# Kernel optimization log

Hardware: AMD Instinct MI355X
Metric: run time of the kernel (lower is better)

## Reference

```python
import jax, jax.numpy as jnp
import numpy as np

B, T, D = 32, 1024, 1024  # batch, t_k (encoder steps), attn_sz == cell_state_sz


def setup_inputs() -> dict:
    key = jax.random.key(0)
    ks = jax.random.split(key, 7)
    scale = 1.0 / np.sqrt(D)
    return {
        "h_i": jax.random.normal(ks[0], (B, T, D), jnp.float32),
        "s_t": jax.random.normal(ks[1], (B, D), jnp.float32),
        "coverage": jax.random.uniform(ks[2], (B, T), jnp.float32),
        "W_h": jax.random.normal(ks[3], (D, D), jnp.float32) * scale,
        "W_s": jax.random.normal(ks[4], (D, D), jnp.float32) * scale,
        "b_s": jnp.zeros((D,), jnp.float32),
        "W_c": jax.random.normal(ks[5], (D,), jnp.float32) * scale,  # Dense(1 -> D) kernel
        "V_w": jax.random.normal(ks[6], (D,), jnp.float32) * scale,  # Dense(D -> 1) kernel
    }


def reference(h_i, s_t, coverage, W_h, W_s, b_s, W_c, V_w):
    # enc_features = W_h(h_i): (B, T, D)
    enc_features = jnp.einsum("btd,de->bte", h_i, W_h)
    # dec_features = W_s(s_t) broadcast over time: (B, 1, D)
    dec_features = (s_t @ W_s + b_s)[:, None, :]
    # coverage features: scalar coverage per step times (1->D) kernel
    cov_features = coverage[:, :, None] * W_c[None, None, :]
    features = enc_features + dec_features + cov_features
    # e_t = V(tanh(features)) squeezed to (B, T)
    e_t = jnp.einsum("btd,d->bt", jnp.tanh(features), V_w)
    a_t = jax.nn.softmax(e_t, axis=1)
    coverage_new = coverage + a_t
    # context = a_t @ h_i : (B, D)
    context_vector = jnp.einsum("bt,btd->bd", a_t, h_i)
    return context_vector, a_t, coverage_new
```

## Files before the change

kernel.cpp:

```cpp
#include <hip/hip_runtime.h>

#define B_ 32
#define T_ 1024
#define D_ 1024
#define M_ (B_ * T_)
#define NT_ 8
#define NT2 4
#define BM_ 128
#define BN_ 128
#define BK_ 64
#define NKT (D_ / BK_)
#define LSTR 72

#define FENCE_ALL() asm volatile("s_waitcnt vmcnt(0) lgkmcnt(0)" ::: "memory")

typedef __attribute__((ext_vector_type(8))) short short8;
typedef __attribute__((ext_vector_type(4))) float f32x4;

__device__ __forceinline__ unsigned f2bf(float f) {
    union { float f; unsigned u; } v; v.f = f;
    return (v.u + 0x7FFFu + ((v.u >> 16) & 1u)) >> 16;
}
__device__ __forceinline__ unsigned pack2(float a, float b) {
    return f2bf(a) | (f2bf(b) << 16);
}
__device__ __forceinline__ float bf2f(unsigned hi16) {
    union { unsigned u; float f; } v; v.u = hi16 << 16;
    return v.f;
}
__device__ __forceinline__ float fast_tanh(float x) {
    x = fminf(15.0f, fmaxf(-15.0f, x));
    float e = __expf(2.0f * x);
    return (e - 1.0f) * __fdividef(1.0f, e + 1.0f);
}

#define PREP_CONVH_BLKS 2048
#define PREP_CONVWT_BLKS 256
#define PREP_DEC_BLKS (B_ * 16)
__global__ __launch_bounds__(256) void prep_kernel(
    const float* __restrict__ h_i, uint4* __restrict__ h_bf4,
    const float* __restrict__ W_h, unsigned short* __restrict__ Wt,
    const float* __restrict__ s_t, const float* __restrict__ W_s,
    const float* __restrict__ b_s, float* __restrict__ dec_part)
{
    __shared__ float smem[64 * 65];
    const int bid = blockIdx.x;
    const int tid = threadIdx.x;
    if (bid < PREP_CONVH_BLKS) {
        const int idx = bid * 256 + tid;
        const int stride = PREP_CONVH_BLKS * 256;
        const int ngroups = M_ * D_ / 8;
        const float4* in4 = (const float4*)h_i;
        for (int g = idx; g < ngroups; g += stride) {
            const float4 a = in4[2 * g];
            const float4 b = in4[2 * g + 1];
            h_bf4[g] = make_uint4(pack2(a.x, a.y), pack2(a.z, a.w),
                                  pack2(b.x, b.y), pack2(b.z, b.w));
        }
    } else if (bid < PREP_CONVH_BLKS + PREP_CONVWT_BLKS) {
        const int tb = bid - PREP_CONVH_BLKS;
        float (*tile)[65] = (float (*)[65])smem;
        const int k0 = (tb & 15) * 64;
        const int n0 = (tb >> 4) * 64;
        const int tx = tid & 63, ty = tid >> 6;
#pragma unroll
        for (int r = 0; r < 16; ++r) {
            const int row = ty * 16 + r;
            tile[row][tx] = W_h[(size_t)(k0 + row) * D_ + n0 + tx];
        }
        __syncthreads();
#pragma unroll
        for (int r = 0; r < 16; ++r) {
            const int row = ty * 16 + r;
            Wt[(size_t)(n0 + row) * D_ + k0 + tx] = (unsigned short)f2bf(tile[tx][row]);
        }
    } else {
        const int db = bid - (PREP_CONVH_BLKS + PREP_CONVWT_BLKS);
        const int kc = db & 3;
        const int nc = (db >> 2) & 3;
        const int b  = db >> 4;
        const int d = nc * 256 + tid;
        const int k0 = kc * 256;
        float* s_lds = smem;
        s_lds[tid] = s_t[b * D_ + k0 + tid];
        __syncthreads();
        float acc = (kc == 0) ? b_s[d] : 0.f;
#pragma unroll 8
        for (int k = 0; k < 256; ++k) acc += s_lds[k] * W_s[(size_t)(k0 + k) * D_ + d];
        dec_part[kc * (B_ * D_) + b * D_ + d] = acc;
    }
}

__global__ __launch_bounds__(512, 2) void attn_gemm2(
    const unsigned short* __restrict__ h_bf, const unsigned short* __restrict__ wt_bf,
    const float* __restrict__ dec_part, const float* __restrict__ coverage,
    const float* __restrict__ W_c, const float* __restrict__ V_w,
    float* __restrict__ e_part)
{
    __shared__ __align__(16) unsigned short lds2[2][2][256 * 64];
    __shared__ float e_red[4][256];

    const int tid = threadIdx.x;
    const int nt2 = blockIdx.x >> 7;
    const int mt  = blockIdx.x & 127;
    const int m0 = mt * 256;
    const int n0 = nt2 * 256;
    const int bb = m0 >> 10;

    const int wave = tid >> 6;
    const int lane = tid & 63;
    const int wr = wave >> 2;
    const int wc = wave & 3;
    const int lr = lane & 15;
    const int lk = lane >> 4;

    f32x4 acc[8][4];
    const f32x4 fzero = {0.f, 0.f, 0.f, 0.f};
#pragma unroll
    for (int i = 0; i < 8; ++i)
#pragma unroll
        for (int j = 0; j < 4; ++j) acc[i][j] = fzero;

    const char* gA = (const char*)h_bf + (size_t)m0 * (D_ * 2);
    const char* gB = (const char*)wt_bf + (size_t)n0 * (D_ * 2);
    const int lrow8 = lane >> 3;
    const int scol = (((lane & 7) ^ lrow8) << 4);
    const int sw = (lr & 7) << 4;

#define STAGE2(buf, kt)                                                            \
    {                                                                              \
        _Pragma("unroll")                                                          \
        for (int j = 0; j < 4; ++j) {                                              \
            const int c = wave * 4 + j;                                            \
            const int row = c * 8 + lrow8;                                         \
            const size_t goff = (size_t)row * (D_ * 2) + (size_t)(kt) * 128 + scol;\
            __builtin_amdgcn_global_load_lds(                                      \
                (const __attribute__((address_space(1))) void*)(gA + goff),        \
                (__attribute__((address_space(3))) void*)((char*)lds2 +            \
                    ((buf) * 2 + 0) * 32768 + c * 1024), 16, 0, 0);                \
            __builtin_amdgcn_global_load_lds(                                      \
                (const __attribute__((address_space(1))) void*)(gB + goff),        \
                (__attribute__((address_space(3))) void*)((char*)lds2 +            \
                    ((buf) * 2 + 1) * 32768 + c * 1024), 16, 0, 0);                \
        }                                                                          \
    }

    STAGE2(0, 0);
    FENCE_ALL();
    __syncthreads();

    short8 aA[4][2];
    short8 bB[4][2];

#define LOADA(g)                                                                   \
    _Pragma("unroll")                                                              \
    for (int mi = 0; mi < 4; ++mi)                                                 \
        _Pragma("unroll")                                                          \
        for (int kk = 0; kk < 2; ++kk)                                             \
            aA[mi][kk] = *(const short8*)(ldsA +                                   \
                (wr * 128 + ((g) * 4 + mi) * 16 + lr) * 128 +                      \
                (((kk) * 64 + lk * 16) ^ sw));

#define LOADB(pair)                                                                \
    _Pragma("unroll")                                                              \
    for (int nn = 0; nn < 2; ++nn)                                                 \
        _Pragma("unroll")                                                          \
        for (int kk = 0; kk < 2; ++kk)                                             \
            bB[(pair) * 2 + nn][kk] = *(const short8*)(ldsB +                      \
                (wc * 64 + ((pair) * 2 + nn) * 16 + lr) * 128 +                    \
                (((kk) * 64 + lk * 16) ^ sw));

#define MFMA_Q(goff, npair)                                                        \
    __builtin_amdgcn_s_setprio(1);                                                 \
    _Pragma("unroll")                                                              \
    for (int mi = 0; mi < 4; ++mi)                                                 \
        _Pragma("unroll")                                                          \
        for (int nn = 0; nn < 2; ++nn)                                             \
            _Pragma("unroll")                                                      \
            for (int kk = 0; kk < 2; ++kk)                                         \
                acc[(goff) + mi][(npair) * 2 + nn] =                               \
                    __builtin_amdgcn_mfma_f32_16x16x32_bf16(                       \
                        aA[mi][kk], bB[(npair) * 2 + nn][kk],                      \
                        acc[(goff) + mi][(npair) * 2 + nn], 0, 0, 0);              \
    __builtin_amdgcn_s_setprio(0);

    for (int kt = 0; kt < NKT; ++kt) {
        const int cur = kt & 1;
        const char* ldsA = (const char*)lds2 + (cur * 2 + 0) * 32768;
        const char* ldsB = (const char*)lds2 + (cur * 2 + 1) * 32768;

        if (kt + 1 < NKT) STAGE2(cur ^ 1, kt + 1);
        LOADA(0);
        LOADB(0);
        MFMA_Q(0, 0);
        __builtin_amdgcn_s_barrier();

        LOADB(1);
        MFMA_Q(0, 1);
        __builtin_amdgcn_s_barrier();

        LOADA(1);
        MFMA_Q(4, 1);
        __builtin_amdgcn_s_barrier();

        MFMA_Q(4, 0);
        FENCE_ALL();
        __syncthreads();
    }
#undef STAGE2
#undef LOADA
#undef LOADB
#undef MFMA_Q

    float esum[8][4];
    float covv[8][4];
#pragma unroll
    for (int mi = 0; mi < 8; ++mi)
#pragma unroll
        for (int r = 0; r < 4; ++r) {
            esum[mi][r] = 0.f;
            covv[mi][r] = coverage[m0 + wr * 128 + mi * 16 + lk * 4 + r];
        }
    const float* dp = dec_part + bb * D_;
#pragma unroll
    for (int ni = 0; ni < 4; ++ni) {
        const int n = n0 + wc * 64 + ni * 16 + lr;
        const float vw = V_w[n];
        const float dc = dp[n] + dp[B_ * D_ + n] + dp[2 * B_ * D_ + n] + dp[3 * B_ * D_ + n];
        const float wcv = W_c[n];
#pragma unroll
        for (int mi = 0; mi < 8; ++mi)
#pragma unroll
            for (int r = 0; r < 4; ++r) {
                const float f = acc[mi][ni][r] + dc + covv[mi][r] * wcv;
                esum[mi][r] += fast_tanh(f) * vw;
            }
    }
#pragma unroll
    for (int off = 1; off <= 8; off <<= 1)
#pragma unroll
        for (int mi = 0; mi < 8; ++mi)
#pragma unroll
            for (int r = 0; r < 4; ++r)
                esum[mi][r] += __shfl_xor(esum[mi][r], off, 64);

    if (lr == 0) {
#pragma unroll
        for (int mi = 0; mi < 8; ++mi)
#pragma unroll
            for (int r = 0; r < 4; ++r)
                e_red[wc][wr * 128 + mi * 16 + lk * 4 + r] = esum[mi][r];
    }
    FENCE_ALL();
    __syncthreads();
    if (tid < 256)
        e_part[(size_t)nt2 * M_ + m0 + tid] =
            e_red[0][tid] + e_red[1][tid] + e_red[2][tid] + e_red[3][tid];
}

__global__ __launch_bounds__(256, 2) void attn_gemm_kernel(
    const float* __restrict__ h_i, const float* __restrict__ W_h,
    const float* __restrict__ dec_part, const float* __restrict__ coverage,
    const float* __restrict__ W_c, const float* __restrict__ V_w,
    float* __restrict__ e_part)
{
    __shared__ __align__(16) unsigned short lA[BM_][LSTR];
    __shared__ __align__(16) unsigned short lB[BN_][LSTR];
    __shared__ float e_red[256];

    const int tid = threadIdx.x;
    const int nt = blockIdx.x >> 8;
    const int mt = blockIdx.x & 255;
    const int m0 = mt * BM_;
    const int n0 = nt * BN_;
    const int bb = m0 >> 10;

    const int wave = tid >> 6;
    const int lane = tid & 63;
    const int wr = wave >> 1, wc = wave & 1;
    const int lr = lane & 15;
    const int lk = lane >> 4;

    f32x4 acc[4][4];
    const f32x4 fzero = {0.f, 0.f, 0.f, 0.f};
#pragma unroll
    for (int i = 0; i < 4; ++i)
#pragma unroll
        for (int j = 0; j < 4; ++j) acc[i][j] = fzero;

    const int a_row = tid >> 4;
    const int a_k = (tid & 15) << 2;
    const float* hA = h_i + (size_t)m0 * D_;

    for (int k0 = 0; k0 < D_; k0 += BK_) {
#pragma unroll
        for (int p = 0; p < 8; ++p) {
            const int row = a_row + p * 16;
            const float4 v = *(const float4*)(hA + (size_t)row * D_ + (k0 + a_k));
            *(uint2*)&lA[row][a_k] = make_uint2(pack2(v.x, v.y), pack2(v.z, v.w));
        }
#pragma unroll
        for (int p = 0; p < 8; ++p) {
            const int task = tid + p * 256;
            const int n = task & 127;
            const int kg = task >> 7;
            const float* wp = W_h + (size_t)(k0 + kg * 4) * D_ + n0 + n;
            const float x0 = wp[0 * D_], x1 = wp[1 * D_], x2 = wp[2 * D_], x3 = wp[3 * D_];
            *(uint2*)&lB[n][kg * 4] = make_uint2(pack2(x0, x1), pack2(x2, x3));
        }
        __syncthreads();

        short8 af[2][4], bfr[2][4];
#pragma unroll
        for (int kk = 0; kk < 2; ++kk)
#pragma unroll
            for (int i = 0; i < 4; ++i) {
                af[kk][i]  = *(const short8*)&lA[wr * 64 + i * 16 + lr][kk * 32 + lk * 8];
                bfr[kk][i] = *(const short8*)&lB[wc * 64 + i * 16 + lr][kk * 32 + lk * 8];
            }
#pragma unroll
        for (int kk = 0; kk < 2; ++kk)
#pragma unroll
            for (int mi = 0; mi < 4; ++mi)
#pragma unroll
                for (int ni = 0; ni < 4; ++ni)
                    acc[mi][ni] = __builtin_amdgcn_mfma_f32_16x16x32_bf16(
                        af[kk][mi], bfr[kk][ni], acc[mi][ni], 0, 0, 0);
        __syncthreads();
    }

    float esum[4][4];
    float covv[4][4];
#pragma unroll
    for (int mi = 0; mi < 4; ++mi)
#pragma unroll
        for (int r = 0; r < 4; ++r) {
            esum[mi][r] = 0.f;
            covv[mi][r] = coverage[m0 + wr * 64 + mi * 16 + lk * 4 + r];
        }
    const float* dp = dec_part + bb * D_;
#pragma unroll
    for (int ni = 0; ni < 4; ++ni) {
        const int n = n0 + wc * 64 + ni * 16 + lr;
        const float vw = V_w[n];
        const float dc = dp[n] + dp[B_ * D_ + n] + dp[2 * B_ * D_ + n] + dp[3 * B_ * D_ + n];
        const float wcv = W_c[n];
#pragma unroll
        for (int mi = 0; mi < 4; ++mi)
#pragma unroll
            for (int r = 0; r < 4; ++r) {
                const float f = acc[mi][ni][r] + dc + covv[mi][r] * wcv;
                esum[mi][r] += fast_tanh(f) * vw;
            }
    }
#pragma unroll
    for (int off = 1; off <= 8; off <<= 1)
#pragma unroll
        for (int mi = 0; mi < 4; ++mi)
#pragma unroll
            for (int r = 0; r < 4; ++r)
                esum[mi][r] += __shfl_xor(esum[mi][r], off, 64);

    if (lr == 0) {
#pragma unroll
        for (int mi = 0; mi < 4; ++mi)
#pragma unroll
            for (int r = 0; r < 4; ++r)
                e_red[wc * 128 + wr * 64 + mi * 16 + lk * 4 + r] = esum[mi][r];
    }
    __syncthreads();
    if (tid < 128)
        e_part[(size_t)nt * M_ + m0 + tid] = e_red[tid] + e_red[128 + tid];
}

__global__ __launch_bounds__(256) void softmax_kernel(
    const float* __restrict__ e_part, const float* __restrict__ coverage,
    float* __restrict__ a_out, float* __restrict__ cov_out,
    float* __restrict__ a_ws, int nparts)
{
    const int b = blockIdx.x;
    const int tid = threadIdx.x;
    __shared__ float redmx[4], redsum[4];
    float e[4];
#pragma unroll
    for (int j = 0; j < 4; ++j) {
        const int t = tid + j * 256;
        float s = 0.f;
        for (int p = 0; p < nparts; ++p) s += e_part[(size_t)p * M_ + b * T_ + t];
        e[j] = s;
    }
    float mx = fmaxf(fmaxf(e[0], e[1]), fmaxf(e[2], e[3]));
#pragma unroll
    for (int off = 32; off > 0; off >>= 1) mx = fmaxf(mx, __shfl_xor(mx, off, 64));
    if ((tid & 63) == 0) redmx[tid >> 6] = mx;
    __syncthreads();
    mx = fmaxf(fmaxf(redmx[0], redmx[1]), fmaxf(redmx[2], redmx[3]));
    float p4[4];
    float ps = 0.f;
#pragma unroll
    for (int j = 0; j < 4; ++j) { p4[j] = __expf(e[j] - mx); ps += p4[j]; }
#pragma unroll
    for (int off = 32; off > 0; off >>= 1) ps += __shfl_xor(ps, off, 64);
    if ((tid & 63) == 0) redsum[tid >> 6] = ps;
    __syncthreads();
    ps = redsum[0] + redsum[1] + redsum[2] + redsum[3];
    const float inv = __fdividef(1.f, ps);
#pragma unroll
    for (int j = 0; j < 4; ++j) {
        const int idx = b * T_ + tid + j * 256;
        const float a = p4[j] * inv;
        a_out[idx] = a;
        a_ws[idx] = a;
        cov_out[idx] = coverage[idx] + a;
    }
}

__global__ __launch_bounds__(256) void ctx_part_bf(
    const unsigned short* __restrict__ h_bf, const float* __restrict__ a_t,
    float* __restrict__ ctx_part)
{
    const int bid = blockIdx.x;
    const int b = bid >> 3;
    const int dc = (bid >> 2) & 1;
    const int tc = bid & 3;
    const int tid = threadIdx.x;
    const int d0 = dc * 512 + tid * 2;
    __shared__ float a_lds[256];
    a_lds[tid] = a_t[b * T_ + tc * 256 + tid];
    __syncthreads();
    const unsigned short* hp = h_bf + ((size_t)(b * T_ + tc * 256)) * D_ + d0;
    float acc0 = 0.f, acc1 = 0.f;
#pragma unroll 8
    for (int t = 0; t < 256; ++t) {
        const unsigned v = *(const unsigned*)(hp + (size_t)t * D_);
        const float a = a_lds[t];
        acc0 += a * bf2f(v & 0xFFFFu);
        acc1 += a * bf2f(v >> 16);
    }
    *(float2*)(ctx_part + tc * (B_ * D_) + b * D_ + d0) = make_float2(acc0, acc1);
}

__global__ __launch_bounds__(256) void ctx_part_f32(
    const float* __restrict__ h_i, const float* __restrict__ a_t,
    float* __restrict__ ctx_part)
{
    const int bid = blockIdx.x;
    const int b = bid >> 4;
    const int dc = (bid >> 2) & 3;
    const int tc = bid & 3;
    const int tid = threadIdx.x;
    const int d = dc * 256 + tid;
    __shared__ float a_lds[256];
    a_lds[tid] = a_t[b * T_ + tc * 256 + tid];
    __syncthreads();
    const float* hp = h_i + ((size_t)(b * T_ + tc * 256)) * D_ + d;
    float acc = 0.f;
#pragma unroll 8
    for (int t = 0; t < 256; ++t) acc += a_lds[t] * hp[(size_t)t * D_];
    ctx_part[tc * (B_ * D_) + b * D_ + d] = acc;
}

__global__ __launch_bounds__(256) void dec_kernel(
    const float* __restrict__ s_t, const float* __restrict__ W_s,
    const float* __restrict__ b_s, float* __restrict__ dec_part)
{
    const int bid = blockIdx.x;
    const int kc = bid & 3;
    const int nc = (bid >> 2) & 3;
    const int b  = bid >> 4;
    const int d = nc * 256 + threadIdx.x;
    const int k0 = kc * 256;
    __shared__ float s_lds[256];
    s_lds[threadIdx.x] = s_t[b * D_ + k0 + threadIdx.x];
    __syncthreads();
    float acc = (kc == 0) ? b_s[d] : 0.f;
#pragma unroll 8
    for (int k = 0; k < 256; ++k) acc += s_lds[k] * W_s[(size_t)(k0 + k) * D_ + d];
    dec_part[kc * (B_ * D_) + b * D_ + d] = acc;
}

__global__ __launch_bounds__(256) void ctx_reduce_kernel(
    const float* __restrict__ ctx_part, float* __restrict__ out)
{
    const int i = blockIdx.x * 256 + threadIdx.x;
    out[i] = ctx_part[i] + ctx_part[B_ * D_ + i] + ctx_part[2 * B_ * D_ + i] +
             ctx_part[3 * B_ * D_ + i];
}

extern "C" void kernel_launch(void* const* d_in, const int* in_sizes, int n_in,
                              void* d_out, int out_size, void* d_ws, size_t ws_size,
                              hipStream_t stream)
{
    (void)in_sizes; (void)n_in; (void)out_size;
    const float* h_i      = (const float*)d_in[0];
    const float* s_t      = (const float*)d_in[1];
    const float* coverage = (const float*)d_in[2];
    const float* W_h      = (const float*)d_in[3];
    const float* W_s      = (const float*)d_in[4];
    const float* b_s      = (const float*)d_in[5];
    const float* W_c      = (const float*)d_in[6];
    const float* V_w      = (const float*)d_in[7];

    float* out     = (float*)d_out;
    float* ctx_out = out;
    float* a_out   = out + B_ * T_;
    float* cov_out = out + 2 * B_ * T_;

    float* ws       = (float*)d_ws;
    float* dec_part = ws;
    float* e_part   = dec_part + 4 * B_ * D_;
    float* ctx_part = e_part + NT_ * M_;
    float* a_ws     = ctx_part + 4 * B_ * D_;
    const size_t f32_count = 8 * (size_t)B_ * D_ + (size_t)NT_ * M_ + (size_t)B_ * T_;
    unsigned short* h_bf  = (unsigned short*)(ws + f32_count);
    unsigned short* wt_bf = h_bf + (size_t)M_ * D_;
    const size_t need = f32_count * 4 + ((size_t)M_ * D_ + (size_t)D_ * D_) * 2;

    if (ws_size >= need) {
        prep_kernel<<<PREP_CONVH_BLKS + PREP_CONVWT_BLKS + PREP_DEC_BLKS, 256, 0, stream>>>(
            h_i, (uint4*)h_bf, W_h, wt_bf, s_t, W_s, b_s, dec_part);
        attn_gemm2<<<NT2 * (M_ / 256), 512, 0, stream>>>(h_bf, wt_bf, dec_part,
                                                         coverage, W_c, V_w, e_part);
        softmax_kernel<<<B_, 256, 0, stream>>>(e_part, coverage, a_out, cov_out, a_ws, NT2);
        ctx_part_bf<<<B_ * 8, 256, 0, stream>>>(h_bf, a_ws, ctx_part);
    } else {
        dec_kernel<<<B_ * 16, 256, 0, stream>>>(s_t, W_s, b_s, dec_part);
        attn_gemm_kernel<<<NT_ * (M_ / BM_), 256, 0, stream>>>(h_i, W_h, dec_part,
                                                               coverage, W_c, V_w, e_part);
        softmax_kernel<<<B_, 256, 0, stream>>>(e_part, coverage, a_out, cov_out, a_ws, NT_);
        ctx_part_f32<<<B_ * 16, 256, 0, stream>>>(h_i, a_ws, ctx_part);
    }
    ctx_reduce_kernel<<<(B_ * D_) / 256, 256, 0, stream>>>(ctx_part, ctx_out);
}
```

Baseline: 161.3 us.

## Interleave next-tile global->LDS loads across four MFMA phases with vmcnt barriers

Restructures the GEMM main loop so the prefetch of the next K-tile is split into per-phase pieces (B low, B high, A quarters) issued between MFMA groups. Each phase waits with partial vmcnt counts plus a barrier, replacing the full vmcnt(0)+syncthreads at the end of every iteration. A fragments are loaded in four smaller groups while B fragments load once per tile. The aim is to keep global loads in flight while MFMAs run and to cut full-drain stalls. In exchange the wave-to-buffer ownership logic is more intricate, and the last iteration issues a redundant wrapped-around load of tile 0.

```diff
diff --git a/kernel.cpp b/kernel.cpp
--- a/kernel.cpp
+++ b/kernel.cpp
@@ -127,90 +127,100 @@
     const int scol = (((lane & 7) ^ lrow8) << 4);
     const int sw = (lr & 7) << 4;
 
-#define STAGE2(buf, kt)                                                            \
+#define GLOAD(mat, chunk, kt, buf)                                                 \
     {                                                                              \
-        _Pragma("unroll")                                                          \
-        for (int j = 0; j < 4; ++j) {                                              \
-            const int c = wave * 4 + j;                                            \
-            const int row = c * 8 + lrow8;                                         \
-            const size_t goff = (size_t)row * (D_ * 2) + (size_t)(kt) * 128 + scol;\
-            __builtin_amdgcn_global_load_lds(                                      \
-                (const __attribute__((address_space(1))) void*)(gA + goff),        \
-                (__attribute__((address_space(3))) void*)((char*)lds2 +            \
-                    ((buf) * 2 + 0) * 32768 + c * 1024), 16, 0, 0);                \
-            __builtin_amdgcn_global_load_lds(                                      \
-                (const __attribute__((address_space(1))) void*)(gB + goff),        \
-                (__attribute__((address_space(3))) void*)((char*)lds2 +            \
-                    ((buf) * 2 + 1) * 32768 + c * 1024), 16, 0, 0);                \
-        }                                                                          \
-    }
-
-    STAGE2(0, 0);
-    FENCE_ALL();
-    __syncthreads();
-
-    short8 aA[4][2];
-    short8 bB[4][2];
+        const int row_ = (chunk) * 8 + lrow8;                                      \
+        const size_t goff_ = (size_t)row_ * (D_ * 2) + (size_t)(kt) * 128 + scol;  \
+        __builtin_amdgcn_global_load_lds(                                          \
+            (const __attribute__((address_space(1))) void*)(((mat) ? gB : gA) + goff_), \
+            (__attribute__((address_space(3))) void*)((char*)lds2 +                \
+                ((buf) * 2 + (mat)) * 32768 + (chunk) * 1024), 16, 0, 0);          \
+    }
+#define ST_BLO(buf, kt) { GLOAD(1, 2 * wave, kt, buf); GLOAD(1, 2 * wave + 1, kt, buf); }
+#define ST_BHI(buf, kt) { GLOAD(1, 16 + 2 * wave, kt, buf); GLOAD(1, 16 + 2 * wave + 1, kt, buf); }
+#define ST_AU(buf, kt, g)                                                          \
+    { const int c_ = (wave < 4) ? ((g) * 4 + wave) : (16 + (g) * 4 + (wave - 4));  \
+      GLOAD(0, c_, kt, buf); }
+
+#define PH_BAR(N)                                                                  \
+    asm volatile("s_waitcnt vmcnt(" #N ")" ::: "memory");                          \
+    __builtin_amdgcn_s_barrier();                                                  \
+    asm volatile("" ::: "memory")
 
 #define LOADA(g)                                                                   \
     _Pragma("unroll")                                                              \
-    for (int mi = 0; mi < 4; ++mi)                                                 \
+    for (int m = 0; m < 2; ++m)                                                    \
         _Pragma("unroll")                                                          \
         for (int kk = 0; kk < 2; ++kk)                                             \
-            aA[mi][kk] = *(const short8*)(ldsA +                                   \
-                (wr * 128 + ((g) * 4 + mi) * 16 + lr) * 128 +                      \
-                (((kk) * 64 + lk * 16) ^ sw));
-
-#define LOADB(pair)                                                                \
-    _Pragma("unroll")                                                              \
-    for (int nn = 0; nn < 2; ++nn)                                                 \
-        _Pragma("unroll")                                                          \
-        for (int kk = 0; kk < 2; ++kk)                                             \
-            bB[(pair) * 2 + nn][kk] = *(const short8*)(ldsB +                      \
-                (wc * 64 + ((pair) * 2 + nn) * 16 + lr) * 128 +                    \
-                (((kk) * 64 + lk * 16) ^ sw));
-
-#define MFMA_Q(goff, npair)                                                        \
+            aA[m][kk] = *(const short8*)(ldsA +                                    \
+                (wr * 128 + ((g) * 2 + m) * 16 + lr) * 128 +                       \
+                ((kk * 64 + lk * 16) ^ sw));
+
+#define MFMAQ(g)                                                                   \
     __builtin_amdgcn_s_setprio(1);                                                 \
     _Pragma("unroll")                                                              \
-    for (int mi = 0; mi < 4; ++mi)                                                 \
+    for (int m = 0; m < 2; ++m)                                                    \
         _Pragma("unroll")                                                          \
-        for (int nn = 0; nn < 2; ++nn)                                             \
+        for (int ni = 0; ni < 4; ++ni)                                             \
             _Pragma("unroll")                                                      \
             for (int kk = 0; kk < 2; ++kk)                                         \
-                acc[(goff) + mi][(npair) * 2 + nn] =                               \
-                    __builtin_amdgcn_mfma_f32_16x16x32_bf16(                       \
-                        aA[mi][kk], bB[(npair) * 2 + nn][kk],                      \
-                        acc[(goff) + mi][(npair) * 2 + nn], 0, 0, 0);              \
+                acc[(g) * 2 + m][ni] = __builtin_amdgcn_mfma_f32_16x16x32_bf16(    \
+                    aA[m][kk], bB[ni][kk], acc[(g) * 2 + m][ni], 0, 0, 0);         \
     __builtin_amdgcn_s_setprio(0);
+
+    ST_BLO(0, 0); ST_BHI(0, 0);
+    ST_AU(0, 0, 0); ST_AU(0, 0, 1); ST_AU(0, 0, 2); ST_AU(0, 0, 3);
+    FENCE_ALL();
+    __syncthreads();
 
     for (int kt = 0; kt < NKT; ++kt) {
         const int cur = kt & 1;
+        const int nxt = cur ^ 1;
+        const int ktn = (kt + 1) & (NKT - 1);
         const char* ldsA = (const char*)lds2 + (cur * 2 + 0) * 32768;
         const char* ldsB = (const char*)lds2 + (cur * 2 + 1) * 32768;
 
-        if (kt + 1 < NKT) STAGE2(cur ^ 1, kt + 1);
+        short8 aA[2][2];
+        short8 bB[4][2];
+
+        PH_BAR(3);
+#pragma unroll
+        for (int ni = 0; ni < 4; ++ni)
+#pragma unroll
+            for (int kk = 0; kk < 2; ++kk)
+                bB[ni][kk] = *(const short8*)(ldsB +
+                    (wc * 64 + ni * 16 + lr) * 128 + ((kk * 64 + lk * 16) ^ sw));
         LOADA(0);
-        LOADB(0);
-        MFMA_Q(0, 0);
-        __builtin_amdgcn_s_barrier();
-
-        LOADB(1);
-        MFMA_Q(0, 1);
-        __builtin_amdgcn_s_barrier();
-
+        ST_BLO(nxt, ktn);
+        MFMAQ(0);
+
+        PH_BAR(4);
         LOADA(1);
-        MFMA_Q(4, 1);
-        __builtin_amdgcn_s_barrier();
-
-        MFMA_Q(4, 0);
-        FENCE_ALL();
-        __syncthreads();
-    }
-#undef STAGE2
+        ST_BHI(nxt, ktn);
+        ST_AU(nxt, ktn, 0);
+        MFMAQ(1);
+
+        PH_BAR(5);
+        LOADA(2);
+        ST_AU(nxt, ktn, 1);
+        ST_AU(nxt, ktn, 2);
+        MFMAQ(2);
+
+        PH_BAR(7);
+        LOADA(3);
+        ST_AU(nxt, ktn, 3);
+        MFMAQ(3);
+    }
+#undef GLOAD
+#undef ST_BLO
+#undef ST_BHI
+#undef ST_AU
+#undef PH_BAR
 #undef LOADA
-#undef LOADB
-#undef MFMA_Q
+#undef MFMAQ
+
+    FENCE_ALL();
+    __syncthreads();
 
     float esum[8][4];
     float covv[8][4];
```

New measurement: 149.7 us. 7.2% less time.
